# Performance work log

Hardware: AMD Instinct MI355X
Metric: run time of the kernel (lower is better)

## Reference

```python
import math
import jax, jax.numpy as jnp
import numpy as np

S, B, IN, D, H, L, F, WIN = 500, 32, 256, 512, 8, 2, 2048, 100


def setup_inputs() -> dict:
    key = jax.random.key(0)
    ks = jax.random.split(key, 20)
    s = 0.02
    inp = {
        "x": jax.random.normal(ks[0], (S, B, IN), dtype=jnp.float32),
        "W_emb": jax.random.normal(ks[1], (IN, D), dtype=jnp.float32) * s,
        "b_emb": jnp.zeros((D,), jnp.float32),
        "Wq": jax.random.normal(ks[2], (L, D, D), dtype=jnp.float32) * s,
        "bq": jnp.zeros((L, D), jnp.float32),
        "Wk": jax.random.normal(ks[3], (L, D, D), dtype=jnp.float32) * s,
        "bk": jnp.zeros((L, D), jnp.float32),
        "Wv": jax.random.normal(ks[4], (L, D, D), dtype=jnp.float32) * s,
        "bv": jnp.zeros((L, D), jnp.float32),
        "Wo": jax.random.normal(ks[5], (L, D, D), dtype=jnp.float32) * s,
        "bo": jnp.zeros((L, D), jnp.float32),
        "ln1_s": jnp.ones((L, D), jnp.float32),
        "ln1_b": jnp.zeros((L, D), jnp.float32),
        "W1": jax.random.normal(ks[6], (L, D, F), dtype=jnp.float32) * s,
        "b1": jnp.zeros((L, F), jnp.float32),
        "W2": jax.random.normal(ks[7], (L, F, D), dtype=jnp.float32) * s,
        "b2": jnp.zeros((L, D), jnp.float32),
        "ln2_s": jnp.ones((L, D), jnp.float32),
        "ln2_b": jnp.zeros((L, D), jnp.float32),
    }
    return inp


def _pos_encoding(seq_len, d_model, dtype):
    pos = jnp.arange(seq_len, dtype=dtype)[:, None]
    div = jnp.exp(jnp.arange(0, d_model, 2, dtype=dtype) * (-math.log(10000.0) / d_model))
    ang = pos * div  # [S, D/2]
    # interleave sin/cos -> pe[:,0::2]=sin, pe[:,1::2]=cos
    return jnp.stack([jnp.sin(ang), jnp.cos(ang)], axis=-1).reshape(seq_len, d_model)


def _layernorm(y, scale, bias, eps=1e-5):
    m = y.mean(-1, keepdims=True)
    v = ((y - m) ** 2).mean(-1, keepdims=True)
    return (y - m) / jnp.sqrt(v + eps) * scale + bias


def reference(x, W_emb, b_emb, Wq, bq, Wk, bk, Wv, bv, Wo, bo,
              ln1_s, ln1_b, W1, b1, W2, b2, ln2_s, ln2_b):
    seq_len, batch, _ = x.shape
    d_model = W_emb.shape[1]
    n_layers = Wq.shape[0]
    hd = d_model // H

    # embedding + positional encoding (dropout is identity in eval mode)
    h = x @ W_emb + b_emb + _pos_encoding(seq_len, d_model, x.dtype)[:, None, :]

    idx = jnp.arange(seq_len)
    diff = idx[:, None] - idx[None, :]
    amask = jnp.where((diff >= 0) & (diff < WIN), 0.0, -jnp.inf).astype(x.dtype)

    for l in range(n_layers):
        # multi-head self-attention (post-norm encoder layer)
        q = (h @ Wq[l] + bq[l]).reshape(seq_len, batch, H, hd)
        k = (h @ Wk[l] + bk[l]).reshape(seq_len, batch, H, hd)
        v = (h @ Wv[l] + bv[l]).reshape(seq_len, batch, H, hd)
        scores = jnp.einsum('ibhd,jbhd->bhij', q, k) / math.sqrt(hd) + amask
        attn = jax.nn.softmax(scores, axis=-1)
        o = jnp.einsum('bhij,jbhd->ibhd', attn, v).reshape(seq_len, batch, d_model)
        h = _layernorm(h + o @ Wo[l] + bo[l], ln1_s[l], ln1_b[l])
        # feed-forward (relu)
        ff = jax.nn.relu(h @ W1[l] + b1[l]) @ W2[l] + b2[l]
        h = _layernorm(h + ff, ln2_s[l], ln2_b[l])
    return h
```

## Files before the change

kernel.cpp:

```cpp
#include <hip/hip_runtime.h>
#include <stdint.h>

#define SEQ   500
#define BATCH 32
#define DIN   256
#define DM    512
#define NH    8
#define NL    2
#define DF    2048
#define WINSZ 100
#define HD    64
#define ROWS  (SEQ*BATCH)
#define MPAD  16128

typedef __bf16 bf16x8 __attribute__((ext_vector_type(8)));
typedef float  f32x4  __attribute__((ext_vector_type(4)));

__device__ __forceinline__ unsigned short bfbits(float f) {
    unsigned int u = __builtin_bit_cast(unsigned int, f);
    u = u + 0x7fffu + ((u >> 16) & 1u);
    return (unsigned short)(u >> 16);
}
__device__ __forceinline__ unsigned int pack2(float a, float b) {
    return (unsigned int)bfbits(a) | ((unsigned int)bfbits(b) << 16);
}
__device__ __forceinline__ float blo(unsigned int u) { return __builtin_bit_cast(float, u << 16); }
__device__ __forceinline__ float bhi(unsigned int u) { return __builtin_bit_cast(float, u & 0xffff0000u); }

__device__ __forceinline__ void async16(void* lds, const void* g) {
    __builtin_amdgcn_global_load_lds((__attribute__((address_space(1))) void*)(void*)g,
                                     (__attribute__((address_space(3))) void*)(void*)lds,
                                     16, 0, 0);
}

__global__ __launch_bounds__(256) void tcast_k(const float* __restrict__ src,
                                               unsigned short* __restrict__ dst,
                                               int R, int C) {
    __shared__ float t[32][33];
    int c0 = blockIdx.x * 32, r0 = blockIdx.y * 32;
    int tx = threadIdx.x, ty = threadIdx.y;
#pragma unroll
    for (int k = 0; k < 32; k += 8)
        t[ty + k][tx] = src[(size_t)(r0 + ty + k) * C + c0 + tx];
    __syncthreads();
#pragma unroll
    for (int k = 0; k < 32; k += 8)
        dst[(size_t)(c0 + ty + k) * R + r0 + tx] = bfbits(t[tx][ty + k]);
}

__global__ __launch_bounds__(256) void prep_k(const float* __restrict__ bq,
                                              const float* __restrict__ bk,
                                              const float* __restrict__ bv,
                                              float* __restrict__ bias_qkv,
                                              float* __restrict__ pe) {
    int tid = blockIdx.x * 256 + threadIdx.x;
    if (tid < SEQ * DM) {
        int s = tid >> 9, c = tid & 511;
        int p = c >> 1;
        float div = expf(-(float)(2 * p) * (9.210340371976184f / 512.0f));
        float ang = (float)s * div;
        pe[tid] = (c & 1) ? cosf(ang) : sinf(ang);
    }
    if (tid < NL * 3 * DM) {
        int l = tid / (3 * DM), r = tid % (3 * DM);
        float v = (r < DM) ? bq[l * DM + r]
                : (r < 2 * DM) ? bk[l * DM + r - DM]
                               : bv[l * DM + r - 2 * DM];
        bias_qkv[tid] = v;
    }
}

__global__ __launch_bounds__(256) void xcast_k(const float* __restrict__ x,
                                               unsigned short* __restrict__ xb, int n) {
    int i = (blockIdx.x * 256 + threadIdx.x) * 4;
    if (i < n) {
        float4 v = *(const float4*)&x[i];
        uint2 o; o.x = pack2(v.x, v.y); o.y = pack2(v.z, v.w);
        *(uint2*)&xb[i] = o;
    }
}

template <int BM, int BN, int MODE>
__global__ __launch_bounds__(256, 2)
void gemm2_k(const unsigned short* __restrict__ A,
             const unsigned short* __restrict__ Wt,
             const float* __restrict__ bias,
             unsigned short* __restrict__ outB,
             const float* __restrict__ pe,
             int Mt, int Nt, int K, int N) {
    constexpr int NTH = 256;
    constexpr int SLOTS = 3;
    constexpr int PD  = 2;
    constexpr int NWC = BN / 64;
    constexpr int MI  = 4;
    constexpr int JSH = 5;

    __shared__ unsigned short LA[SLOTS][BM * 32];
    __shared__ unsigned short LB[SLOTS][BN * 32];

    const int tid = threadIdx.x, lane = tid & 63, wid = tid >> 6;
    const int wr = wid / NWC, wc = wid % NWC;
    const int lr = lane & 15, grp = lane >> 4;

    int lin = blockIdx.x;
    int base_m = (lin / (8 * Nt)) * 8;
    int Gc = min(8, Mt - base_m);
    int rem = lin - base_m * Nt;
    int mt = base_m + rem % Gc, nt = rem / Gc;
    const int m0 = mt * BM, n0 = nt * BN;

    const int NKT = K >> 5;

    auto stageA = [&](int kt, int part) {
        int slot = kt % SLOTS, k0 = kt << 5;
        int g = part * NTH + tid;
        int row = g >> 2, c = g & 3;
        int src = c ^ ((row >> 1) & 3);
        async16(&LA[slot][g * 8], A + (size_t)(m0 + row) * K + k0 + src * 8);
    };
    auto stageB = [&](int kt, int part) {
        int slot = kt % SLOTS, k0 = kt << 5;
        int g = part * NTH + tid;
        int pos = g >> 2, cs = g & 3;
        int j   = pos >> JSH;
        int wcc = (pos >> 4) & (NWC - 1);
        int lrr = pos & 15;
        int rb  = wcc * 64 + lrr * 4 + j;
        int c   = cs ^ ((rb >> 3) & 3);
        async16(&LB[slot][g * 8], Wt + (size_t)(n0 + rb) * K + k0 + c * 8);
    };

    f32x4 acc[MI][4] = {};

#pragma unroll
    for (int t = 0; t < PD; ++t) {
        stageA(t, 0); stageA(t, 1); stageB(t, 0); stageB(t, 1);
    }

    for (int kt = 0; kt < NKT; ++kt) {
        const int slot = kt % SLOTS;
        const bool pf = (kt + PD < NKT);
        if (kt + 1 < NKT)      asm volatile("s_waitcnt vmcnt(4)" ::: "memory");
        else                   asm volatile("s_waitcnt vmcnt(0)" ::: "memory");
        __builtin_amdgcn_s_barrier();
        __builtin_amdgcn_sched_barrier(0);

        const int bxor = grp ^ ((lr >> 1) & 3);
        bf16x8 af[MI], bf[4];

#pragma unroll
        for (int i = 0; i < MI; ++i) {
            int ra = wr * (MI * 16) + i * 16 + lr;
            af[i] = *(const bf16x8*)&LA[slot][ra * 32 + ((grp ^ ((ra >> 1) & 3)) << 3)];
        }
#pragma unroll
        for (int j = 0; j < 2; ++j) {
            int pos = j * (16 * NWC) + wc * 16 + lr;
            bf[j] = *(const bf16x8*)&LB[slot][(pos * 4 + bxor) * 8];
        }
        if (pf) { stageA(kt + PD, 0); stageA(kt + PD, 1); }
        __builtin_amdgcn_s_setprio(1);
#pragma unroll
        for (int i = 0; i < MI; ++i)
#pragma unroll
            for (int j = 0; j < 2; ++j)
                acc[i][j] = __builtin_amdgcn_mfma_f32_16x16x32_bf16(af[i], bf[j], acc[i][j], 0, 0, 0);
        __builtin_amdgcn_s_setprio(0);
        __builtin_amdgcn_s_barrier();
        __builtin_amdgcn_sched_barrier(0);

#pragma unroll
        for (int j = 2; j < 4; ++j) {
            int pos = j * (16 * NWC) + wc * 16 + lr;
            bf[j] = *(const bf16x8*)&LB[slot][(pos * 4 + bxor) * 8];
        }
        if (pf) { stageB(kt + PD, 0); stageB(kt + PD, 1); }
        __builtin_amdgcn_s_setprio(1);
#pragma unroll
        for (int i = 0; i < MI; ++i)
#pragma unroll
            for (int j = 2; j < 4; ++j)
                acc[i][j] = __builtin_amdgcn_mfma_f32_16x16x32_bf16(af[i], bf[j], acc[i][j], 0, 0, 0);
        __builtin_amdgcn_s_setprio(0);
        __builtin_amdgcn_s_barrier();
        __builtin_amdgcn_sched_barrier(0);
    }

    const int colb = n0 + wc * 64 + lr * 4;
    float4 bv4 = *(const float4*)&bias[colb];
#pragma unroll
    for (int i = 0; i < MI; ++i) {
#pragma unroll
        for (int v = 0; v < 4; ++v) {
            int row = m0 + wr * (MI * 16) + i * 16 + grp * 4 + v;
            float f0 = acc[i][0][v] + bv4.x;
            float f1 = acc[i][1][v] + bv4.y;
            float f2 = acc[i][2][v] + bv4.z;
            float f3 = acc[i][3][v] + bv4.w;
            if (MODE == 2) {
                f0 = fmaxf(f0, 0.f); f1 = fmaxf(f1, 0.f);
                f2 = fmaxf(f2, 0.f); f3 = fmaxf(f3, 0.f);
            }
            if (MODE == 3) {
                int s = min(row >> 5, SEQ - 1);
                float4 p4 = *(const float4*)&pe[(size_t)s * DM + colb];
                f0 += p4.x; f1 += p4.y; f2 += p4.z; f3 += p4.w;
            }
            uint2 wv; wv.x = pack2(f0, f1); wv.y = pack2(f2, f3);
            *(uint2*)&outB[(size_t)row * N + colb] = wv;
        }
    }
}

template <int MODE>
__global__ __launch_bounds__(512, 2)
void gemm3_k(const unsigned short* __restrict__ A,
             const unsigned short* __restrict__ Wt,
             const float* __restrict__ bias,
             unsigned short* __restrict__ outB,
             int Mt, int Nt, int K, int N) {
    __shared__ unsigned short LA[2][256 * 64];
    __shared__ unsigned short LB[2][256 * 64];

    const int tid = threadIdx.x, lane = tid & 63, wid = tid >> 6;
    const int wr = wid >> 2, wc = wid & 3;
    const int lr = lane & 15, grp = lane >> 4;

    int lin = blockIdx.x;
    int base_m = (lin / (8 * Nt)) * 8;
    int Gc = min(8, Mt - base_m);
    int rem = lin - base_m * Nt;
    int mt = base_m + rem % Gc, nt = rem / Gc;
    const int m0 = mt * 256, n0 = nt * 256;

    const int NKT = K >> 6;

    auto stA = [&](int kt, int part) {
        int slot = kt & 1, k0 = kt << 6;
        int g = part * 512 + tid;
        int row = g >> 3, c = g & 7;
        int src = c ^ (row & 7);
        async16(&LA[slot][g * 8], A + (size_t)(m0 + row) * K + k0 + src * 8);
    };
    auto stB = [&](int kt, int part) {
        int slot = kt & 1, k0 = kt << 6;
        int g = part * 512 + tid;
        int pos = g >> 3, cs = g & 7;
        int j = pos >> 6, wcc = (pos >> 4) & 3, lrr = pos & 15;
        int rb = wcc * 64 + lrr * 4 + j;
        int c = cs ^ (lrr & 7);
        async16(&LB[slot][g * 8], Wt + (size_t)(n0 + rb) * K + k0 + c * 8);
    };

    f32x4 acc[8][4] = {};

    stB(0, 0); stB(0, 1); stA(0, 0); stA(0, 2); stB(0, 2); stB(0, 3); stA(0, 1); stA(0, 3);

    for (int kt = 0; kt < NKT; ++kt) {
        const int slot = kt & 1;
        const bool pf = (kt + 1 < NKT);
        bf16x8 afL[8], afH[8], bf01[4], bf23[4];

        asm volatile("s_waitcnt vmcnt(4)" ::: "memory");
        __builtin_amdgcn_s_barrier();
        __builtin_amdgcn_sched_barrier(0);
#pragma unroll
        for (int j = 0; j < 2; ++j)
#pragma unroll
            for (int kk = 0; kk < 2; ++kk) {
                int pos = j * 64 + wc * 16 + lr;
                bf01[j * 2 + kk] = *(const bf16x8*)&LB[slot][pos * 64 + (((kk * 4 + grp) ^ (lr & 7)) << 3)];
            }
#pragma unroll
        for (int i = 0; i < 4; ++i)
#pragma unroll
            for (int kk = 0; kk < 2; ++kk) {
                int ra = wr * 128 + i * 16 + lr;
                afL[i * 2 + kk] = *(const bf16x8*)&LA[slot][ra * 64 + (((kk * 4 + grp) ^ (ra & 7)) << 3)];
            }
        if (pf) { stB(kt + 1, 0); stB(kt + 1, 1); }
        __builtin_amdgcn_s_setprio(1);
#pragma unroll
        for (int i = 0; i < 4; ++i)
#pragma unroll
            for (int j = 0; j < 2; ++j)
#pragma unroll
                for (int kk = 0; kk < 2; ++kk)
                    acc[i][j] = __builtin_amdgcn_mfma_f32_16x16x32_bf16(afL[i * 2 + kk], bf01[j * 2 + kk], acc[i][j], 0, 0, 0);
        __builtin_amdgcn_s_setprio(0);
        __builtin_amdgcn_sched_barrier(0);

        if (pf) asm volatile("s_waitcnt vmcnt(4)" ::: "memory");
        else    asm volatile("s_waitcnt vmcnt(2)" ::: "memory");
        __builtin_amdgcn_s_barrier();
        __builtin_amdgcn_sched_barrier(0);
#pragma unroll
        for (int j = 0; j < 2; ++j)
#pragma unroll
            for (int kk = 0; kk < 2; ++kk) {
                int pos = (2 + j) * 64 + wc * 16 + lr;
                bf23[j * 2 + kk] = *(const bf16x8*)&LB[slot][pos * 64 + (((kk * 4 + grp) ^ (lr & 7)) << 3)];
            }
        if (pf) { stA(kt + 1, 0); stA(kt + 1, 2); }
        __builtin_amdgcn_s_setprio(1);
#pragma unroll
        for (int i = 0; i < 4; ++i)
#pragma unroll
            for (int j = 0; j < 2; ++j)
#pragma unroll
                for (int kk = 0; kk < 2; ++kk)
                    acc[i][2 + j] = __builtin_amdgcn_mfma_f32_16x16x32_bf16(afL[i * 2 + kk], bf23[j * 2 + kk], acc[i][2 + j], 0, 0, 0);
        __builtin_amdgcn_s_setprio(0);
        __builtin_amdgcn_sched_barrier(0);

        if (pf) asm volatile("s_waitcnt vmcnt(4)" ::: "memory");
        else    asm volatile("s_waitcnt vmcnt(0)" ::: "memory");
        __builtin_amdgcn_s_barrier();
        __builtin_amdgcn_sched_barrier(0);
#pragma unroll
        for (int i = 0; i < 4; ++i)
#pragma unroll
            for (int kk = 0; kk < 2; ++kk) {
                int ra = wr * 128 + (4 + i) * 16 + lr;
                afH[i * 2 + kk] = *(const bf16x8*)&LA[slot][ra * 64 + (((kk * 4 + grp) ^ (ra & 7)) << 3)];
            }
        if (pf) { stB(kt + 1, 2); stB(kt + 1, 3); }
        __builtin_amdgcn_s_setprio(1);
#pragma unroll
        for (int i = 0; i < 4; ++i)
#pragma unroll
            for (int j = 0; j < 2; ++j)
#pragma unroll
                for (int kk = 0; kk < 2; ++kk)
                    acc[4 + i][j] = __builtin_amdgcn_mfma_f32_16x16x32_bf16(afH[i * 2 + kk], bf01[j * 2 + kk], acc[4 + i][j], 0, 0, 0);
        __builtin_amdgcn_s_setprio(0);
        __builtin_amdgcn_sched_barrier(0);

        __builtin_amdgcn_s_barrier();
        __builtin_amdgcn_sched_barrier(0);
        if (pf) { stA(kt + 1, 1); stA(kt + 1, 3); }
        __builtin_amdgcn_s_setprio(1);
#pragma unroll
        for (int i = 0; i < 4; ++i)
#pragma unroll
            for (int j = 0; j < 2; ++j)
#pragma unroll
                for (int kk = 0; kk < 2; ++kk)
                    acc[4 + i][2 + j] = __builtin_amdgcn_mfma_f32_16x16x32_bf16(afH[i * 2 + kk], bf23[j * 2 + kk], acc[4 + i][2 + j], 0, 0, 0);
        __builtin_amdgcn_s_setprio(0);
        __builtin_amdgcn_sched_barrier(0);
    }

    const int colb = n0 + wc * 64 + lr * 4;
    float4 bv4 = *(const float4*)&bias[colb];
#pragma unroll
    for (int i = 0; i < 8; ++i) {
#pragma unroll
        for (int v = 0; v < 4; ++v) {
            int row = m0 + wr * 128 + i * 16 + grp * 4 + v;
            float f0 = acc[i][0][v] + bv4.x;
            float f1 = acc[i][1][v] + bv4.y;
            float f2 = acc[i][2][v] + bv4.z;
            float f3 = acc[i][3][v] + bv4.w;
            if (MODE == 2) {
                f0 = fmaxf(f0, 0.f); f1 = fmaxf(f1, 0.f);
                f2 = fmaxf(f2, 0.f); f3 = fmaxf(f3, 0.f);
            }
            uint2 wv; wv.x = pack2(f0, f1); wv.y = pack2(f2, f3);
            *(uint2*)&outB[(size_t)row * N + colb] = wv;
        }
    }
}

__global__ __launch_bounds__(256) void vtrans_k(const unsigned short* __restrict__ qkv,
                                                unsigned short* __restrict__ vT) {
    __shared__ unsigned short t[32][72];
    const int s0 = blockIdx.x * 32;
    const int bh = blockIdx.y;
    const int b = bh >> 3, h = bh & 7;
    const int tid = threadIdx.x;
    {
        int sl = tid >> 3;
        int c  = tid & 7;
        int s  = s0 + sl;
        uint4 val = {0, 0, 0, 0};
        if (s < SEQ)
            val = *(const uint4*)&qkv[(size_t)(s * BATCH + b) * (3 * DM) + 2 * DM + h * HD + c * 8];
        *(uint4*)&t[sl][c * 8] = val;
    }
    __syncthreads();
    {
        int d  = tid >> 2;
        int s8 = (tid & 3) * 8;
        unsigned short v[8];
#pragma unroll
        for (int j = 0; j < 8; ++j) v[j] = t[s8 + j][d];
        *(uint4*)&vT[(size_t)(bh * 64 + d) * 512 + s0 + s8] = *(uint4*)v;
    }
}

#define QBLK  64
#define NIB   8
#define KTIL  11
#define KSTR  72
#define VSTR  200
#define PSTR  200

__global__ __launch_bounds__(256, 3) void attn_k(const unsigned short* __restrict__ qkv,
                                                 const unsigned short* __restrict__ vT,
                                                 unsigned short* __restrict__ ob) {
    __shared__ unsigned short KV[12800];
    __shared__ unsigned short Pl[64 * PSTR];

    const int ib = blockIdx.x & (NIB - 1), bh = blockIdx.x >> 3;
    const int b = bh >> 3, h = bh & 7;
    const int i0 = ib * QBLK;
    const int jbase = max(0, i0 - (WINSZ - 1));
    const int jend  = min(SEQ - 1, i0 + QBLK - 1);
    const int nkeys = jend - jbase + 1;
    const int NT  = (nkeys + 15) >> 4;
    const int NKS = (nkeys + 31) >> 5;
    const int tid = threadIdx.x, lane = tid & 63, w = tid >> 6;
    const int q15 = lane & 15, grp = lane >> 4;

#pragma unroll
    for (int it = 0; it < 6; ++it) {
        int g = it * 256 + tid;
        if (g < 1408) {
            int row = g >> 3, c = g & 7;
            uint4 val = {0, 0, 0, 0};
            if (row < nkeys)
                val = *(const uint4*)&qkv[(size_t)((jbase + row) * BATCH + b) * (3 * DM)
                                          + DM + h * HD + c * 8];
            *(uint4*)&KV[row * KSTR + c * 8] = val;
        }
    }
#pragma unroll
    for (int it = 0; it < 7; ++it) {
        int g = it * 256 + tid;
        if (g < 1600) { uint4 z = {0, 0, 0, 0}; *(uint4*)&Pl[g * 8] = z; }
    }
    uint4 vreg[6];
#pragma unroll
    for (int it = 0; it < 6; ++it) {
        int g = it * 256 + tid;
        int r = g / 24, c = g - r * 24;
        uint4 val = {0, 0, 0, 0};
        if (c * 8 < nkeys && jbase + c * 8 + 8 <= 512)
            val = *(const uint4*)&vT[(size_t)(bh * 64 + r) * 512 + jbase + c * 8];
        vreg[it] = val;
    }
    bf16x8 qav, qbv;
    {
        int iq = min(i0 + w * 16 + q15, SEQ - 1);
        size_t qrow = (size_t)(iq * BATCH + b) * (3 * DM) + h * HD;
        uint4 a = *(const uint4*)&qkv[qrow + grp * 8];
        uint4 c = *(const uint4*)&qkv[qrow + 32 + grp * 8];
        qav = __builtin_bit_cast(bf16x8, a);
        qbv = __builtin_bit_cast(bf16x8, c);
    }
    __syncthreads();

    const int i = i0 + w * 16 + q15;
    float sc[KTIL][4];
#pragma unroll
    for (int t = 0; t < KTIL; ++t) {
        if (t >= NT) continue;
        f32x4 acc = {};
        int row = t * 16 + q15;
        bf16x8 kf0 = *(const bf16x8*)&KV[row * KSTR + grp * 8];
        acc = __builtin_amdgcn_mfma_f32_16x16x32_bf16(kf0, qav, acc, 0, 0, 0);
        bf16x8 kf1 = *(const bf16x8*)&KV[row * KSTR + 32 + grp * 8];
        acc = __builtin_amdgcn_mfma_f32_16x16x32_bf16(kf1, qbv, acc, 0, 0, 0);
#pragma unroll
        for (int v = 0; v < 4; ++v) {
            int key = jbase + t * 16 + grp * 4 + v;
            bool valid = (key <= i) && (key > i - WINSZ);
            sc[t][v] = valid ? acc[v] * 0.125f : -1e30f;
        }
    }
    float m = -1e30f;
#pragma unroll
    for (int t = 0; t < KTIL; ++t) {
        if (t >= NT) continue;
#pragma unroll
        for (int v = 0; v < 4; ++v) m = fmaxf(m, sc[t][v]);
    }
    m = fmaxf(m, __shfl_xor(m, 16));
    m = fmaxf(m, __shfl_xor(m, 32));
    float sum = 0.f;
#pragma unroll
    for (int t = 0; t < KTIL; ++t) {
        if (t >= NT) continue;
#pragma unroll
        for (int v = 0; v < 4; ++v) {
            float p = __expf(sc[t][v] - m);
            sc[t][v] = p;
            sum += p;
        }
    }
    sum += __shfl_xor(sum, 16);
    sum += __shfl_xor(sum, 32);

    __syncthreads();

#pragma unroll
    for (int it = 0; it < 6; ++it) {
        int g = it * 256 + tid;
        int r = g / 24, c = g - r * 24;
        *(uint4*)&KV[r * VSTR + c * 8] = vreg[it];
    }
#pragma unroll
    for (int t = 0; t < KTIL; ++t) {
        if (t >= NT) continue;
        uint2 pk;
        pk.x = pack2(sc[t][0], sc[t][1]);
        pk.y = pack2(sc[t][2], sc[t][3]);
        *(uint2*)&Pl[(w * 16 + q15) * PSTR + t * 16 + grp * 4] = pk;
    }
    __syncthreads();

    f32x4 oacc[4] = {};
#pragma unroll
    for (int ks = 0; ks < 6; ++ks) {
        if (ks >= NKS) continue;
        bf16x8 pf = *(const bf16x8*)&Pl[(w * 16 + q15) * PSTR + ks * 32 + grp * 8];
#pragma unroll
        for (int dt = 0; dt < 4; ++dt) {
            bf16x8 vf = *(const bf16x8*)&KV[(dt * 16 + q15) * VSTR + ks * 32 + grp * 8];
            oacc[dt] = __builtin_amdgcn_mfma_f32_16x16x32_bf16(pf, vf, oacc[dt], 0, 0, 0);
        }
    }

#pragma unroll
    for (int v = 0; v < 4; ++v) {
        float rsv = 1.0f / __shfl(sum, grp * 4 + v);
        int irow = i0 + w * 16 + grp * 4 + v;
        if (irow < SEQ) {
            size_t base = (size_t)(irow * BATCH + b) * DM + h * HD + q15;
#pragma unroll
            for (int dt = 0; dt < 4; ++dt)
                ob[base + dt * 16] = bfbits(oacc[dt][v] * rsv);
        }
    }
}

template <int FOUT>
__global__ __launch_bounds__(256) void ln_k(const unsigned short* __restrict__ hin,
                                            const unsigned short* __restrict__ yin,
                                            const float* __restrict__ sc,
                                            const float* __restrict__ bi,
                                            unsigned short* __restrict__ hb,
                                            float* __restrict__ fout) {
    int row = blockIdx.x * 4 + (threadIdx.x >> 6);
    int lane = threadIdx.x & 63;
    size_t base = (size_t)row * DM + lane * 8;
    uint4 hw = *(const uint4*)&hin[base];
    uint4 yw = *(const uint4*)&yin[base];
    float x[8] = {blo(hw.x) + blo(yw.x), bhi(hw.x) + bhi(yw.x),
                  blo(hw.y) + blo(yw.y), bhi(hw.y) + bhi(yw.y),
                  blo(hw.z) + blo(yw.z), bhi(hw.z) + bhi(yw.z),
                  blo(hw.w) + blo(yw.w), bhi(hw.w) + bhi(yw.w)};
    float s = 0.f;
#pragma unroll
    for (int k = 0; k < 8; ++k) s += x[k];
#pragma unroll
    for (int off = 32; off; off >>= 1) s += __shfl_xor(s, off);
    float mean = s * (1.f / DM);
    float q = 0.f;
#pragma unroll
    for (int k = 0; k < 8; ++k) { float d = x[k] - mean; q = fmaf(d, d, q); }
#pragma unroll
    for (int off = 32; off; off >>= 1) q += __shfl_xor(q, off);
    float rstd = rsqrtf(q * (1.f / DM) + 1e-5f);
    float4 s0 = *(const float4*)&sc[lane * 8], s1 = *(const float4*)&sc[lane * 8 + 4];
    float4 b0 = *(const float4*)&bi[lane * 8], b1 = *(const float4*)&bi[lane * 8 + 4];
    float o[8];
    o[0] = (x[0] - mean) * rstd * s0.x + b0.x;  o[1] = (x[1] - mean) * rstd * s0.y + b0.y;
    o[2] = (x[2] - mean) * rstd * s0.z + b0.z;  o[3] = (x[3] - mean) * rstd * s0.w + b0.w;
    o[4] = (x[4] - mean) * rstd * s1.x + b1.x;  o[5] = (x[5] - mean) * rstd * s1.y + b1.y;
    o[6] = (x[6] - mean) * rstd * s1.z + b1.z;  o[7] = (x[7] - mean) * rstd * s1.w + b1.w;
    if (FOUT) {
        float4 w0 = {o[0], o[1], o[2], o[3]}, w1 = {o[4], o[5], o[6], o[7]};
        *(float4*)&fout[base] = w0;
        *(float4*)&fout[base + 4] = w1;
    } else {
        uint4 pk = {pack2(o[0], o[1]), pack2(o[2], o[3]), pack2(o[4], o[5]), pack2(o[6], o[7])};
        *(uint4*)&hb[base] = pk;
    }
}

extern "C" void kernel_launch(void* const* d_in, const int* in_sizes, int n_in,
                              void* d_out, int out_size, void* d_ws, size_t ws_size,
                              hipStream_t stream) {
    const float* x     = (const float*)d_in[0];
    const float* Wemb  = (const float*)d_in[1];
    const float* bemb  = (const float*)d_in[2];
    const float* Wq    = (const float*)d_in[3];
    const float* bq    = (const float*)d_in[4];
    const float* Wk    = (const float*)d_in[5];
    const float* bk    = (const float*)d_in[6];
    const float* Wv    = (const float*)d_in[7];
    const float* bv    = (const float*)d_in[8];
    const float* Wo    = (const float*)d_in[9];
    const float* bo    = (const float*)d_in[10];
    const float* ln1s  = (const float*)d_in[11];
    const float* ln1b  = (const float*)d_in[12];
    const float* W1    = (const float*)d_in[13];
    const float* b1    = (const float*)d_in[14];
    const float* W2    = (const float*)d_in[15];
    const float* b2    = (const float*)d_in[16];
    const float* ln2s  = (const float*)d_in[17];
    const float* ln2b  = (const float*)d_in[18];

    char* p = (char*)d_ws;
    auto carve = [&](size_t bytes) { char* r = p; p += (bytes + 255) & ~(size_t)255; return r; };

    unsigned short* wt_emb = (unsigned short*)carve((size_t)DM * DIN * 2);
    unsigned short* wt_qkv = (unsigned short*)carve((size_t)NL * 3 * DM * DM * 2);
    unsigned short* wt_o   = (unsigned short*)carve((size_t)NL * DM * DM * 2);
    unsigned short* wt_1   = (unsigned short*)carve((size_t)NL * DF * DM * 2);
    unsigned short* wt_2   = (unsigned short*)carve((size_t)NL * DM * DF * 2);
    float*          biasq  = (float*)carve((size_t)NL * 3 * DM * 4);
    float*          pe     = (float*)carve((size_t)SEQ * DM * 4);
    unsigned short* xb     = (unsigned short*)carve((size_t)MPAD * DIN * 2);
    unsigned short* h      = (unsigned short*)carve((size_t)MPAD * DM * 2);
    unsigned short* ob     = (unsigned short*)carve((size_t)MPAD * DM * 2);
    unsigned short* t0b    = (unsigned short*)carve((size_t)MPAD * DM * 2);
    unsigned short* vT     = (unsigned short*)carve((size_t)BATCH * NH * 64 * 512 * 2 + 1024);
    unsigned short* qkv    = (unsigned short*)carve((size_t)MPAD * DF * 2);
    unsigned short* f1     = qkv;

    dim3 blk256(256);

    tcast_k<<<dim3(DM / 32, DIN / 32), dim3(32, 8), 0, stream>>>(Wemb, wt_emb, DIN, DM);
    for (int l = 0; l < NL; ++l) {
        tcast_k<<<dim3(DM / 32, DM / 32), dim3(32, 8), 0, stream>>>(Wq + (size_t)l * DM * DM, wt_qkv + (size_t)l * 3 * DM * DM, DM, DM);
        tcast_k<<<dim3(DM / 32, DM / 32), dim3(32, 8), 0, stream>>>(Wk + (size_t)l * DM * DM, wt_qkv + (size_t)l * 3 * DM * DM + (size_t)DM * DM, DM, DM);
        tcast_k<<<dim3(DM / 32, DM / 32), dim3(32, 8), 0, stream>>>(Wv + (size_t)l * DM * DM, wt_qkv + (size_t)l * 3 * DM * DM + (size_t)2 * DM * DM, DM, DM);
        tcast_k<<<dim3(DM / 32, DM / 32), dim3(32, 8), 0, stream>>>(Wo + (size_t)l * DM * DM, wt_o + (size_t)l * DM * DM, DM, DM);
        tcast_k<<<dim3(DF / 32, DM / 32), dim3(32, 8), 0, stream>>>(W1 + (size_t)l * DM * DF, wt_1 + (size_t)l * DF * DM, DM, DF);
        tcast_k<<<dim3(DM / 32, DF / 32), dim3(32, 8), 0, stream>>>(W2 + (size_t)l * DF * DM, wt_2 + (size_t)l * DM * DF, DF, DM);
    }
    prep_k<<<dim3((SEQ * DM + 255) / 256), blk256, 0, stream>>>(bq, bk, bv, biasq, pe);
    xcast_k<<<dim3(ROWS * DIN / 4 / 256), blk256, 0, stream>>>(x, xb, ROWS * DIN);

    const int Mt256 = MPAD / 256;
    const int Mt128 = MPAD / 128;

    gemm2_k<128, 128, 3><<<dim3(Mt128 * 4), blk256, 0, stream>>>(
        xb, wt_emb, bemb, h, pe, Mt128, 4, DIN, DM);

    for (int l = 0; l < NL; ++l) {
        gemm2_k<128, 128, 1><<<dim3(Mt128 * 12), blk256, 0, stream>>>(
            h, wt_qkv + (size_t)l * 3 * DM * DM, biasq + (size_t)l * 3 * DM,
            qkv, nullptr, Mt128, 12, DM, 3 * DM);
        vtrans_k<<<dim3(16, BATCH * NH), blk256, 0, stream>>>(qkv, vT);
        attn_k<<<dim3(BATCH * NH * NIB), blk256, 0, stream>>>(qkv, vT, ob);
        gemm2_k<128, 128, 1><<<dim3(Mt128 * 4), blk256, 0, stream>>>(
            ob, wt_o + (size_t)l * DM * DM, bo + (size_t)l * DM,
            t0b, nullptr, Mt128, 4, DM, DM);
        ln_k<0><<<dim3(ROWS / 4), blk256, 0, stream>>>(h, t0b, ln1s + (size_t)l * DM, ln1b + (size_t)l * DM, h, nullptr);
        gemm3_k<2><<<dim3(Mt256 * 8), dim3(512), 0, stream>>>(
            h, wt_1 + (size_t)l * DF * DM, b1 + (size_t)l * DF,
            f1, Mt256, 8, DM, DF);
        gemm2_k<128, 128, 1><<<dim3(Mt128 * 4), blk256, 0, stream>>>(
            f1, wt_2 + (size_t)l * DM * DF, b2 + (size_t)l * DM,
            t0b, nullptr, Mt128, 4, DF, DM);
        if (l == NL - 1)
            ln_k<1><<<dim3(ROWS / 4), blk256, 0, stream>>>(h, t0b, ln2s + (size_t)l * DM, ln2b + (size_t)l * DM, nullptr, (float*)d_out);
        else
            ln_k<0><<<dim3(ROWS / 4), blk256, 0, stream>>>(h, t0b, ln2s + (size_t)l * DM, ln2b + (size_t)l * DM, h, nullptr);
    }
}
```

Before: 416.9 us.

## Replace 3-slot K32 GEMM with double-buffered K64 four-quadrant pipelined GEMM

Replaces the 128x128 GEMM kernel, which used a 3-slot K=32 LDS ring, with a 2-slot ring over K=64 tiles. The swizzle is widened to 8 chunks and the main loop is split into four MFMA quadrant phases. Each phase prefetches a quarter of the next tile's A or B data, so global loads interleave with compute and the number of barriers per unit of K drops. The cost is more LDS per block (64 KB versus 48 KB), which may limit occupancy, and a more fragile vmcnt accounting scheme.

```diff
diff --git a/kernel.cpp b/kernel.cpp
--- a/kernel.cpp
+++ b/kernel.cpp
@@ -80,26 +80,19 @@
     }
 }
 
-template <int BM, int BN, int MODE>
+template <int MODE>
 __global__ __launch_bounds__(256, 2)
-void gemm2_k(const unsigned short* __restrict__ A,
+void gemm4_k(const unsigned short* __restrict__ A,
              const unsigned short* __restrict__ Wt,
              const float* __restrict__ bias,
              unsigned short* __restrict__ outB,
              const float* __restrict__ pe,
              int Mt, int Nt, int K, int N) {
-    constexpr int NTH = 256;
-    constexpr int SLOTS = 3;
-    constexpr int PD  = 2;
-    constexpr int NWC = BN / 64;
-    constexpr int MI  = 4;
-    constexpr int JSH = 5;
-
-    __shared__ unsigned short LA[SLOTS][BM * 32];
-    __shared__ unsigned short LB[SLOTS][BN * 32];
+    __shared__ unsigned short LA[2][128 * 64];
+    __shared__ unsigned short LB[2][128 * 64];
 
     const int tid = threadIdx.x, lane = tid & 63, wid = tid >> 6;
-    const int wr = wid / NWC, wc = wid % NWC;
+    const int wr = wid >> 1, wc = wid & 1;
     const int lr = lane & 15, grp = lane >> 4;
 
     int lin = blockIdx.x;
@@ -107,92 +100,133 @@
     int Gc = min(8, Mt - base_m);
     int rem = lin - base_m * Nt;
     int mt = base_m + rem % Gc, nt = rem / Gc;
-    const int m0 = mt * BM, n0 = nt * BN;
-
-    const int NKT = K >> 5;
-
-    auto stageA = [&](int kt, int part) {
-        int slot = kt % SLOTS, k0 = kt << 5;
-        int g = part * NTH + tid;
-        int row = g >> 2, c = g & 3;
-        int src = c ^ ((row >> 1) & 3);
+    const int m0 = mt * 128, n0 = nt * 128;
+
+    const int NKT = K >> 6;
+
+    auto stA = [&](int kt, int part) {
+        int slot = kt & 1, k0 = kt << 6;
+        int g = part * 256 + tid;
+        int row = g >> 3, c = g & 7;
+        int src = c ^ (row & 7);
         async16(&LA[slot][g * 8], A + (size_t)(m0 + row) * K + k0 + src * 8);
     };
-    auto stageB = [&](int kt, int part) {
-        int slot = kt % SLOTS, k0 = kt << 5;
-        int g = part * NTH + tid;
-        int pos = g >> 2, cs = g & 3;
-        int j   = pos >> JSH;
-        int wcc = (pos >> 4) & (NWC - 1);
-        int lrr = pos & 15;
-        int rb  = wcc * 64 + lrr * 4 + j;
-        int c   = cs ^ ((rb >> 3) & 3);
+    auto stB = [&](int kt, int part) {
+        int slot = kt & 1, k0 = kt << 6;
+        int g = part * 256 + tid;
+        int pos = g >> 3, cs = g & 7;
+        int j = pos >> 5, wcc = (pos >> 4) & 1, lrr = pos & 15;
+        int rb = wcc * 64 + lrr * 4 + j;
+        int c = cs ^ (lrr & 7);
         async16(&LB[slot][g * 8], Wt + (size_t)(n0 + rb) * K + k0 + c * 8);
     };
 
-    f32x4 acc[MI][4] = {};
-
-#pragma unroll
-    for (int t = 0; t < PD; ++t) {
-        stageA(t, 0); stageA(t, 1); stageB(t, 0); stageB(t, 1);
-    }
+    f32x4 acc[4][4] = {};
+
+    stB(0, 0); stB(0, 1); stA(0, 0); stA(0, 2); stB(0, 2); stB(0, 3); stA(0, 1); stA(0, 3);
 
     for (int kt = 0; kt < NKT; ++kt) {
-        const int slot = kt % SLOTS;
-        const bool pf = (kt + PD < NKT);
-        if (kt + 1 < NKT)      asm volatile("s_waitcnt vmcnt(4)" ::: "memory");
-        else                   asm volatile("s_waitcnt vmcnt(0)" ::: "memory");
+        const int slot = kt & 1;
+        const bool pf = (kt + 1 < NKT);
+        bf16x8 afL[4], afH[4], bf01[4], bf23[4];
+
+        asm volatile("s_waitcnt vmcnt(4)" ::: "memory");
         __builtin_amdgcn_s_barrier();
         __builtin_amdgcn_sched_barrier(0);
-
-        const int bxor = grp ^ ((lr >> 1) & 3);
-        bf16x8 af[MI], bf[4];
-
-#pragma unroll
-        for (int i = 0; i < MI; ++i) {
-            int ra = wr * (MI * 16) + i * 16 + lr;
-            af[i] = *(const bf16x8*)&LA[slot][ra * 32 + ((grp ^ ((ra >> 1) & 3)) << 3)];
-        }
-#pragma unroll
-        for (int j = 0; j < 2; ++j) {
-            int pos = j * (16 * NWC) + wc * 16 + lr;
-            bf[j] = *(const bf16x8*)&LB[slot][(pos * 4 + bxor) * 8];
-        }
-        if (pf) { stageA(kt + PD, 0); stageA(kt + PD, 1); }
+#pragma unroll
+        for (int j = 0; j < 2; ++j)
+#pragma unroll
+            for (int kk = 0; kk < 2; ++kk) {
+                int pos = j * 32 + wc * 16 + lr;
+                bf01[j * 2 + kk] = *(const bf16x8*)&LB[slot][pos * 64 + (((kk * 4 + grp) ^ (lr & 7)) << 3)];
+            }
+#pragma unroll
+        for (int i = 0; i < 2; ++i)
+#pragma unroll
+            for (int kk = 0; kk < 2; ++kk) {
+                int ra = wr * 64 + i * 16 + lr;
+                afL[i * 2 + kk] = *(const bf16x8*)&LA[slot][ra * 64 + (((kk * 4 + grp) ^ (ra & 7)) << 3)];
+            }
+        if (pf) { stB(kt + 1, 0); stB(kt + 1, 1); }
         __builtin_amdgcn_s_setprio(1);
 #pragma unroll
-        for (int i = 0; i < MI; ++i)
+        for (int i = 0; i < 2; ++i)
 #pragma unroll
             for (int j = 0; j < 2; ++j)
-                acc[i][j] = __builtin_amdgcn_mfma_f32_16x16x32_bf16(af[i], bf[j], acc[i][j], 0, 0, 0);
+#pragma unroll
+                for (int kk = 0; kk < 2; ++kk)
+                    acc[i][j] = __builtin_amdgcn_mfma_f32_16x16x32_bf16(afL[i * 2 + kk], bf01[j * 2 + kk], acc[i][j], 0, 0, 0);
         __builtin_amdgcn_s_setprio(0);
+        __builtin_amdgcn_sched_barrier(0);
+
+        if (pf) asm volatile("s_waitcnt vmcnt(4)" ::: "memory");
+        else    asm volatile("s_waitcnt vmcnt(2)" ::: "memory");
         __builtin_amdgcn_s_barrier();
         __builtin_amdgcn_sched_barrier(0);
-
-#pragma unroll
-        for (int j = 2; j < 4; ++j) {
-            int pos = j * (16 * NWC) + wc * 16 + lr;
-            bf[j] = *(const bf16x8*)&LB[slot][(pos * 4 + bxor) * 8];
-        }
-        if (pf) { stageB(kt + PD, 0); stageB(kt + PD, 1); }
+#pragma unroll
+        for (int j = 0; j < 2; ++j)
+#pragma unroll
+            for (int kk = 0; kk < 2; ++kk) {
+                int pos = (2 + j) * 32 + wc * 16 + lr;
+                bf23[j * 2 + kk] = *(const bf16x8*)&LB[slot][pos * 64 + (((kk * 4 + grp) ^ (lr & 7)) << 3)];
+            }
+        if (pf) { stA(kt + 1, 0); stA(kt + 1, 2); }
         __builtin_amdgcn_s_setprio(1);
 #pragma unroll
-        for (int i = 0; i < MI; ++i)
-#pragma unroll
-            for (int j = 2; j < 4; ++j)
-                acc[i][j] = __builtin_amdgcn_mfma_f32_16x16x32_bf16(af[i], bf[j], acc[i][j], 0, 0, 0);
+        for (int i = 0; i < 2; ++i)
+#pragma unroll
+            for (int j = 0; j < 2; ++j)
+#pragma unroll
+                for (int kk = 0; kk < 2; ++kk)
+                    acc[i][2 + j] = __builtin_amdgcn_mfma_f32_16x16x32_bf16(afL[i * 2 + kk], bf23[j * 2 + kk], acc[i][2 + j], 0, 0, 0);
         __builtin_amdgcn_s_setprio(0);
+        __builtin_amdgcn_sched_barrier(0);
+
+        if (pf) asm volatile("s_waitcnt vmcnt(4)" ::: "memory");
+        else    asm volatile("s_waitcnt vmcnt(0)" ::: "memory");
         __builtin_amdgcn_s_barrier();
+        __builtin_amdgcn_sched_barrier(0);
+#pragma unroll
+        for (int i = 0; i < 2; ++i)
+#pragma unroll
+            for (int kk = 0; kk < 2; ++kk) {
+                int ra = wr * 64 + (2 + i) * 16 + lr;
+                afH[i * 2 + kk] = *(const bf16x8*)&LA[slot][ra * 64 + (((kk * 4 + grp) ^ (ra & 7)) << 3)];
+            }
+        if (pf) { stB(kt + 1, 2); stB(kt + 1, 3); }
+        __builtin_amdgcn_s_setprio(1);
+#pragma unroll
+        for (int i = 0; i < 2; ++i)
+#pragma unroll
+            for (int j = 0; j < 2; ++j)
+#pragma unroll
+                for (int kk = 0; kk < 2; ++kk)
+                    acc[2 + i][j] = __builtin_amdgcn_mfma_f32_16x16x32_bf16(afH[i * 2 + kk], bf01[j * 2 + kk], acc[2 + i][j], 0, 0, 0);
+        __builtin_amdgcn_s_setprio(0);
+        __builtin_amdgcn_sched_barrier(0);
+
+        __builtin_amdgcn_s_barrier();
+        __builtin_amdgcn_sched_barrier(0);
+        if (pf) { stA(kt + 1, 1); stA(kt + 1, 3); }
+        __builtin_amdgcn_s_setprio(1);
+#pragma unroll
+        for (int i = 0; i < 2; ++i)
+#pragma unroll
+            for (int j = 0; j < 2; ++j)
+#pragma unroll
+                for (int kk = 0; kk < 2; ++kk)
+                    acc[2 + i][2 + j] = __builtin_amdgcn_mfma_f32_16x16x32_bf16(afH[i * 2 + kk], bf23[j * 2 + kk], acc[2 + i][2 + j], 0, 0, 0);
+        __builtin_amdgcn_s_setprio(0);
         __builtin_amdgcn_sched_barrier(0);
     }
 
     const int colb = n0 + wc * 64 + lr * 4;
     float4 bv4 = *(const float4*)&bias[colb];
 #pragma unroll
-    for (int i = 0; i < MI; ++i) {
+    for (int i = 0; i < 4; ++i) {
 #pragma unroll
         for (int v = 0; v < 4; ++v) {
-            int row = m0 + wr * (MI * 16) + i * 16 + grp * 4 + v;
+            int row = m0 + wr * 64 + i * 16 + grp * 4 + v;
             float f0 = acc[i][0][v] + bv4.x;
             float f1 = acc[i][1][v] + bv4.y;
             float f2 = acc[i][2][v] + bv4.z;
@@ -648,23 +682,23 @@
     const int Mt256 = MPAD / 256;
     const int Mt128 = MPAD / 128;
 
-    gemm2_k<128, 128, 3><<<dim3(Mt128 * 4), blk256, 0, stream>>>(
+    gemm4_k<3><<<dim3(Mt128 * 4), blk256, 0, stream>>>(
         xb, wt_emb, bemb, h, pe, Mt128, 4, DIN, DM);
 
     for (int l = 0; l < NL; ++l) {
-        gemm2_k<128, 128, 1><<<dim3(Mt128 * 12), blk256, 0, stream>>>(
+        gemm4_k<1><<<dim3(Mt128 * 12), blk256, 0, stream>>>(
             h, wt_qkv + (size_t)l * 3 * DM * DM, biasq + (size_t)l * 3 * DM,
             qkv, nullptr, Mt128, 12, DM, 3 * DM);
         vtrans_k<<<dim3(16, BATCH * NH), blk256, 0, stream>>>(qkv, vT);
         attn_k<<<dim3(BATCH * NH * NIB), blk256, 0, stream>>>(qkv, vT, ob);
-        gemm2_k<128, 128, 1><<<dim3(Mt128 * 4), blk256, 0, stream>>>(
+        gemm4_k<1><<<dim3(Mt128 * 4), blk256, 0, stream>>>(
             ob, wt_o + (size_t)l * DM * DM, bo + (size_t)l * DM,
             t0b, nullptr, Mt128, 4, DM, DM);
         ln_k<0><<<dim3(ROWS / 4), blk256, 0, stream>>>(h, t0b, ln1s + (size_t)l * DM, ln1b + (size_t)l * DM, h, nullptr);
         gemm3_k<2><<<dim3(Mt256 * 8), dim3(512), 0, stream>>>(
             h, wt_1 + (size_t)l * DF * DM, b1 + (size_t)l * DF,
             f1, Mt256, 8, DM, DF);
-        gemm2_k<128, 128, 1><<<dim3(Mt128 * 4), blk256, 0, stream>>>(
+        gemm4_k<1><<<dim3(Mt128 * 4), blk256, 0, stream>>>(
             f1, wt_2 + (size_t)l * DM * DF, b2 + (size_t)l * DM,
             t0b, nullptr, Mt128, 4, DF, DM);
         if (l == NL - 1)
```

Measured after the change: 429.7 us. 3.1% more time.
